# Kernel optimization log

Hardware: AMD Instinct MI355X
Metric: run time of the kernel (lower is better)

Reference implementation:

```python
import jax, jax.numpy as jnp
import numpy as np

DIM = 1024
HEADS = 16
HEAD_DIM = DIM // HEADS
SCALE = HEAD_DIM ** -0.5


def setup_inputs() -> dict:
    key = jax.random.key(0)
    ks = jax.random.split(key, 5)
    B, N, C = 2, 2048, DIM
    x = jax.random.normal(ks[0], (B, N, C), dtype=jnp.float32)
    x2 = jax.random.normal(ks[1], (B, N, C), dtype=jnp.float32)
    # torch nn.Linear weights: [out_features, in_features], no bias (qkv_bias=False)
    s = (1.0 / C) ** 0.5
    Wq = jax.random.uniform(ks[2], (C, C), jnp.float32, -s, s)
    Wa = jax.random.uniform(ks[3], (C, C), jnp.float32, -s, s)
    Wkv = jax.random.uniform(ks[4], (2 * C, C), jnp.float32, -s, s)
    return {"x": x, "x2": x2, "Wq": Wq, "Wa": Wa, "Wkv": Wkv}


def reference(x, x2, Wq, Wa, Wkv):
    B, N, C = x.shape
    H, D = HEADS, HEAD_DIM

    def heads(t):  # [B,N,C] -> [B,H,N,D]
        return t.reshape(B, N, H, D).transpose(0, 2, 1, 3)

    q = heads(x @ Wq.T)
    A = heads(x2 @ Wa.T)
    kv = (x @ Wkv.T).reshape(B, N, 2, H, D).transpose(2, 0, 3, 1, 4)
    k, v = kv[0], kv[1]

    # cascaded double attention (dropout layers in eval mode = identity)
    ATT_q = jax.nn.softmax(jnp.einsum('bhnd,bhmd->bhnm', q, A) * SCALE, axis=-1)
    ATT_k = jax.nn.softmax(jnp.einsum('bhnd,bhmd->bhnm', A, k) * SCALE, axis=-1)
    out = jnp.einsum('bhnm,bhmd->bhnd', ATT_q,
                     jnp.einsum('bhnm,bhmd->bhnd', ATT_k, v))
    return out.transpose(0, 2, 1, 3).reshape(B, N, C)
```

## Files before the change

kernel.cpp:

```cpp
#include <hip/hip_runtime.h>

#define DIM 1024
#define HEADS 16
#define HDIM 64
#define SEQ 2048
#define SCLOG2 0.18033688011112042f

typedef __attribute__((ext_vector_type(8))) short short8;
typedef __attribute__((ext_vector_type(4))) float f32x4;
typedef __attribute__((ext_vector_type(16))) float f32x16;
typedef __attribute__((ext_vector_type(4))) int i32x4;

static __device__ __forceinline__ unsigned short f2bf(float f){
  union { float f; unsigned int u; } v; v.f = f;
  unsigned int r = v.u + 0x7fffu + ((v.u >> 16) & 1u);
  return (unsigned short)(r >> 16);
}

static __device__ __forceinline__ int cvtpk(float lo, float hi){
  int r;
  asm("v_cvt_pk_bf16_f32 %0, %1, %2" : "=v"(r) : "v"(lo), "v"(hi));
  return r;
}
static __device__ __forceinline__ void swap32(int& a, int& b){
  asm("v_permlane32_swap_b32 %0, %1" : "+v"(a), "+v"(b));
}

__device__ __forceinline__ void gl_lds16(const unsigned short* g, unsigned short* l){
  __builtin_amdgcn_global_load_lds((const __attribute__((address_space(1))) void*)g,
                                   (__attribute__((address_space(3))) void*)l, 16, 0, 0);
}

#define CAST_TOTAL 3145728

__global__ __launch_bounds__(256)
void cast_all(const float* __restrict__ x, const float* __restrict__ x2,
              const float* __restrict__ wq, const float* __restrict__ wa,
              const float* __restrict__ wkv, unsigned short* __restrict__ out)
{
  for (int i = blockIdx.x*256 + threadIdx.x; i < CAST_TOTAL; i += gridDim.x*256){
    const float* src; int off;
    if      (i < 1048576){ src = x;   off = i; }
    else if (i < 2097152){ src = x2;  off = i - 1048576; }
    else if (i < 2359296){ src = wq;  off = i - 2097152; }
    else if (i < 2621440){ src = wa;  off = i - 2359296; }
    else                 { src = wkv; off = i - 2621440; }
    float4 v = ((const float4*)src)[off];
    ushort4 o;
    o.x = f2bf(v.x); o.y = f2bf(v.y); o.z = f2bf(v.z); o.w = f2bf(v.w);
    ((ushort4*)out)[i] = o;
  }
}

#define GK 1024

__global__ __launch_bounds__(256)
void gemm_all(const unsigned short* __restrict__ xb,  const unsigned short* __restrict__ x2b,
              const unsigned short* __restrict__ Wqb, const unsigned short* __restrict__ Wab,
              const unsigned short* __restrict__ Wkvb,
              unsigned short* __restrict__ Qw, unsigned short* __restrict__ Aw,
              unsigned short* __restrict__ Kw, unsigned short* __restrict__ Vwt)
{
  __shared__ unsigned short Ald[2][128*64];
  __shared__ unsigned short Bld[2][128*64];
  const int tid  = threadIdx.x;
  const int lane = tid & 63;
  const int wid  = tid >> 6;
  const int l15 = lane & 15, l4 = lane >> 4;
  const int wm = wid >> 1, wn = wid & 1;

  const int bid = blockIdx.x;
  const unsigned short *Abuf, *Bbuf;
  int mbase, nbase, isA;
  if (bid < 768){
    int xcd = bid & 7, s = bid >> 3;
    int mb = xcd*4 + (s & 3);
    int nb = s >> 2;
    nbase = nb*128; mbase = mb*128; isA = 0;
    Abuf = xb;
    Bbuf = (nbase < 1024) ? (Wqb + (size_t)nbase*GK) : (Wkvb + (size_t)(nbase-1024)*GK);
  } else {
    int b2 = bid - 768;
    int xcd = b2 & 7, s = b2 >> 3;
    int mb = xcd*4 + (s & 3);
    int nb = s >> 2;
    nbase = nb*128; mbase = mb*128; isA = 1;
    Abuf = x2b;
    Bbuf = Wab + (size_t)nbase*GK;
  }
  const bool isV = (!isA) && (nbase >= 2048);

  const int srow = wid*32 + (lane >> 3);
  const int scol = ((lane & 7) ^ (lane >> 3)) * 8;
  const unsigned short* gA = Abuf + (size_t)(mbase + srow)*GK + scol;
  const unsigned short* gB = Bbuf + (size_t)srow*GK + scol;

  const int rsw = (l15 & 7) * 8;

  f32x4 acc[4][4];
  #pragma unroll
  for (int i=0;i<4;i++)
    #pragma unroll
    for(int j=0;j<4;j++) acc[i][j] = (f32x4){0.f,0.f,0.f,0.f};

  #pragma unroll
  for (int i=0;i<4;++i){
    gl_lds16(gA + (size_t)(i*8)*GK, &Ald[0][(wid*32 + i*8)*64]);
    gl_lds16(gB + (size_t)(i*8)*GK, &Bld[0][(wid*32 + i*8)*64]);
  }
  asm volatile("s_waitcnt vmcnt(0)" ::: "memory");
  __builtin_amdgcn_s_barrier();
  __builtin_amdgcn_sched_barrier(0);

  for (int t = 0; t < 16; ++t){
    const int cur = t & 1;
    if (t+1 < 16){
      const int nxt = cur ^ 1;
      const int kt = (t+1)*64;
      #pragma unroll
      for (int i=0;i<4;++i){
        gl_lds16(gA + (size_t)(i*8)*GK + kt, &Ald[nxt][(wid*32 + i*8)*64]);
        gl_lds16(gB + (size_t)(i*8)*GK + kt, &Bld[nxt][(wid*32 + i*8)*64]);
      }
    }
    #pragma unroll
    for (int kc = 0; kc < 2; ++kc){
      short8 af[4], bf[4];
      #pragma unroll
      for (int mt=0; mt<4; ++mt)
        af[mt] = *(const short8*)(&Ald[cur][(wm*64 + mt*16 + l15)*64 + ((kc*32 + l4*8) ^ rsw)]);
      #pragma unroll
      for (int nt=0; nt<4; ++nt)
        bf[nt] = *(const short8*)(&Bld[cur][(wn*64 + nt*16 + l15)*64 + ((kc*32 + l4*8) ^ rsw)]);
      __builtin_amdgcn_s_setprio(1);
      if (isV){
        #pragma unroll
        for (int mt=0; mt<4; ++mt)
          #pragma unroll
          for (int nt=0; nt<4; ++nt)
            acc[mt][nt] = __builtin_amdgcn_mfma_f32_16x16x32_bf16(af[mt], bf[nt], acc[mt][nt], 0,0,0);
      } else {
        #pragma unroll
        for (int mt=0; mt<4; ++mt)
          #pragma unroll
          for (int nt=0; nt<4; ++nt)
            acc[mt][nt] = __builtin_amdgcn_mfma_f32_16x16x32_bf16(bf[nt], af[mt], acc[mt][nt], 0,0,0);
      }
      __builtin_amdgcn_s_setprio(0);
    }
    asm volatile("s_waitcnt vmcnt(0)" ::: "memory");
    __builtin_amdgcn_s_barrier();
    __builtin_amdgcn_sched_barrier(0);
  }

  if (!isV){
    unsigned short* dst = isA ? Aw : (nbase < 1024 ? Qw : Kw);
    const int coff = (!isA && nbase >= 1024) ? 1024 : 0;
    const float scale = isA ? SCLOG2 : 1.0f;
    #pragma unroll
    for (int mt=0; mt<4; ++mt){
      int token = mbase + wm*64 + mt*16 + l15;
      int b = token >> 11, n = token & 2047;
      #pragma unroll
      for (int nt=0; nt<4; ++nt){
        int colb = nbase - coff + wn*64 + nt*16 + l4*4;
        int h = colb >> 6, d = colb & 63;
        ushort4 pk;
        pk.x = f2bf(acc[mt][nt][0] * scale);
        pk.y = f2bf(acc[mt][nt][1] * scale);
        pk.z = f2bf(acc[mt][nt][2] * scale);
        pk.w = f2bf(acc[mt][nt][3] * scale);
        *(ushort4*)(dst + ((size_t)((b*HEADS + h)*SEQ + n))*HDIM + d) = pk;
      }
    }
  } else {
    #pragma unroll
    for (int mt=0; mt<4; ++mt){
      int mrow = mbase + wm*64 + mt*16 + l4*4;
      int b = mrow >> 11, nblk = mrow & 2047;
      #pragma unroll
      for (int nt=0; nt<4; ++nt){
        int col = nbase + wn*64 + nt*16 + l15;
        int c2 = col - 2048, h = c2 >> 6, d = c2 & 63;
        ushort4 pk;
        pk.x = f2bf(acc[mt][nt][0]);
        pk.y = f2bf(acc[mt][nt][1]);
        pk.z = f2bf(acc[mt][nt][2]);
        pk.w = f2bf(acc[mt][nt][3]);
        *(ushort4*)(Vwt + ((size_t)((b*HEADS + h)*HDIM + d))*SEQ + nblk) = pk;
      }
    }
  }
}

#define KT2 32
#define NTH 32

__global__ __launch_bounds__(512)
void attn_pass(const unsigned short* __restrict__ Qb,
               const unsigned short* __restrict__ Kb,
               const unsigned short* __restrict__ Vtb,
               unsigned short* __restrict__ ytb,
               float* __restrict__ outf,
               int mode)
{
  __shared__ __align__(16) char SHRAW[65536];
  unsigned short* SH = (unsigned short*)SHRAW;
  const int tid = threadIdx.x, lane = tid & 63, wid = tid >> 6;
  const int l31 = lane & 31, l5 = lane >> 5;
  const int qw = wid & 3, kvh = wid >> 2;

  const int bid = blockIdx.x;
  const int cx = bid & 7, j = bid >> 3;
  const int bh = cx*4 + (j >> 4);
  const int qb = j & 15;
  const int q0 = qb*128 + qw*32;
  const size_t base = (size_t)bh * SEQ * HDIM;

  short8 qf[4];
  #pragma unroll
  for (int db=0; db<4; ++db)
    qf[db] = *(const short8*)(Qb + base + (size_t)(q0 + l31)*HDIM + db*16 + l5*8);

  const unsigned short* gsrc[2];
  int ldst[2];
  int sstep;
  const int grpoff = kvh * 16384;
  if (qw < 2){
    #pragma unroll
    for (int f=0; f<2; ++f){
      gsrc[f] = Kb + base + (size_t)(kvh*1024 + l31)*HDIM + (qw*2 + f)*16 + l5*8;
      ldst[f] = grpoff + (qw*2 + f)*512;
    }
    sstep = KT2*HDIM;
  } else {
    const int db2 = qw - 2;
    #pragma unroll
    for (int f=0; f<2; ++f){
      gsrc[f] = Vtb + base + (size_t)(db2*32 + l31)*SEQ + kvh*1024 + f*16 + l5*8;
      ldst[f] = grpoff + 2048 + (db2*2 + f)*512;
    }
    sstep = KT2;
  }

  f32x16 oo0, oo1, ssum;
  #pragma unroll
  for (int r=0;r<16;++r){ oo0[r]=0.f; oo1[r]=0.f; ssum[r]=0.f; }
  short8 ones;
  #pragma unroll
  for (int jj=0;jj<8;++jj) ones[jj] = (short)0x3F80;

  #pragma unroll
  for (int b=0; b<3; ++b)
    #pragma unroll
    for (int f=0; f<2; ++f)
      gl_lds16(gsrc[f] + (size_t)b*sstep, SH + ldst[f] + b*4096);
  asm volatile("s_waitcnt vmcnt(4)" ::: "memory");
  __builtin_amdgcn_s_barrier();
  __builtin_amdgcn_sched_barrier(0);

  for (int t = 0; t < NTH; ++t){
    if (t+3 < NTH){
      const int pb = ((t+3) & 3) * 4096;
      #pragma unroll
      for (int f=0; f<2; ++f)
        gl_lds16(gsrc[f] + (size_t)(t+3)*sstep, SH + ldst[f] + pb);
    }
    const unsigned short* Kc = SH + grpoff + (t & 3)*4096;
    const unsigned short* Vc = Kc + 2048;

    f32x16 sacc;
    #pragma unroll
    for (int r=0;r<16;++r) sacc[r]=0.f;
    __builtin_amdgcn_s_setprio(1);
    #pragma unroll
    for (int db=0; db<4; ++db){
      short8 kfr = *(const short8*)(Kc + db*512 + lane*8);
      sacc = __builtin_amdgcn_mfma_f32_32x32x16_bf16(kfr, qf[db], sacc, 0,0,0);
    }
    __builtin_amdgcn_s_setprio(0);
    float p[16];
    #pragma unroll
    for (int r=0;r<16;++r)
      p[r] = __builtin_amdgcn_exp2f(sacc[r]);

    #pragma unroll
    for (int kb2=0; kb2<2; ++kb2){
      const int pb2 = kb2*8;
      int a0 = cvtpk(p[pb2+0], p[pb2+1]);
      int b0 = cvtpk(p[pb2+4], p[pb2+5]);
      int a1 = cvtpk(p[pb2+2], p[pb2+3]);
      int b1 = cvtpk(p[pb2+6], p[pb2+7]);
      swap32(a0, b0);
      swap32(a1, b1);
      i32x4 pav; pav[0]=a0; pav[1]=a1; pav[2]=b0; pav[3]=b1;
      short8 paf = *(short8*)&pav;
      __builtin_amdgcn_s_setprio(1);
      ssum = __builtin_amdgcn_mfma_f32_32x32x16_bf16(ones, paf, ssum, 0,0,0);
      short8 v0 = *(const short8*)(Vc + (0*2+kb2)*512 + lane*8);
      oo0 = __builtin_amdgcn_mfma_f32_32x32x16_bf16(v0, paf, oo0, 0,0,0);
      short8 v1 = *(const short8*)(Vc + (1*2+kb2)*512 + lane*8);
      oo1 = __builtin_amdgcn_mfma_f32_32x32x16_bf16(v1, paf, oo1, 0,0,0);
      __builtin_amdgcn_s_setprio(0);
    }

    if (t < NTH-3){
      asm volatile("s_waitcnt vmcnt(4)" ::: "memory");
    } else if (t == NTH-3){
      asm volatile("s_waitcnt vmcnt(2)" ::: "memory");
    } else if (t == NTH-2){
      asm volatile("s_waitcnt vmcnt(0)" ::: "memory");
    }
    __builtin_amdgcn_s_barrier();
    __builtin_amdgcn_sched_barrier(0);
  }

  float* Of  = (float*)SHRAW;
  float* Os1 = (float*)(SHRAW + 128*68*4);
  const int ql = qw*32 + l31;

  if (kvh == 1){
    #pragma unroll
    for (int g=0; g<4; ++g){
      f32x4 w0, w1;
      #pragma unroll
      for (int r=0;r<4;++r){ w0[r] = oo0[g*4+r]; w1[r] = oo1[g*4+r]; }
      int d0 = 8*g + 4*l5;
      *(f32x4*)(Of + ql*68 + d0)      = w0;
      *(f32x4*)(Of + ql*68 + d0 + 32) = w1;
    }
    Os1[ql] = ssum[0];
  }
  __syncthreads();

  if (kvh == 0){
    const float rinv = 1.0f / (ssum[0] + Os1[ql]);
    if (mode == 0){
      #pragma unroll
      for (int r=0;r<16;++r){
        int d0 = (r&3) + 8*(r>>2) + 4*l5;
        float f0 = (oo0[r] + Of[ql*68 + d0])      * rinv;
        float f1 = (oo1[r] + Of[ql*68 + d0 + 32]) * rinv;
        ytb[base + (size_t)(d0)*SEQ + q0 + l31]    = f2bf(f0);
        ytb[base + (size_t)(d0+32)*SEQ + q0 + l31] = f2bf(f1);
      }
    } else {
      #pragma unroll
      for (int g=0; g<4; ++g){
        int d0 = 8*g + 4*l5;
        f32x4 w0 = *(const f32x4*)(Of + ql*68 + d0);
        f32x4 w1 = *(const f32x4*)(Of + ql*68 + d0 + 32);
        #pragma unroll
        for (int r=0;r<4;++r){ w0[r] = (w0[r]+oo0[g*4+r])*rinv; w1[r] = (w1[r]+oo1[g*4+r])*rinv; }
        *(f32x4*)(Of + ql*68 + d0)      = w0;
        *(f32x4*)(Of + ql*68 + d0 + 32) = w1;
      }
    }
  }

  if (mode == 1){
    __syncthreads();
    const int b = bh >> 4, h = bh & 15;
    const int qr = tid >> 2, dh = (tid & 3)*16;
    const float* src = Of + qr*68 + dh;
    float* drow = outf + ((size_t)(b*SEQ + qb*128 + qr))*DIM + h*HDIM + dh;
    #pragma unroll
    for (int k2=0;k2<4;++k2)
      *(float4*)(drow + k2*4) = *(const float4*)(src + k2*4);
  }
}

extern "C" void kernel_launch(void* const* d_in, const int* in_sizes, int n_in,
                              void* d_out, int out_size, void* d_ws, size_t ws_size,
                              hipStream_t stream) {
  const float* x   = (const float*)d_in[0];
  const float* x2  = (const float*)d_in[1];
  const float* Wq  = (const float*)d_in[2];
  const float* Wa  = (const float*)d_in[3];
  const float* Wkv = (const float*)d_in[4];
  float* out = (float*)d_out;

  unsigned short* ws = (unsigned short*)d_ws;
  unsigned short* xb   = ws;
  unsigned short* x2b  = xb   + 4096*1024;
  unsigned short* Wqb  = x2b  + 4096*1024;
  unsigned short* Wab  = Wqb  + 1024*1024;
  unsigned short* Wkvb = Wab  + 1024*1024;
  unsigned short* Qw   = Wkvb + 2048*1024;
  unsigned short* Aw   = Qw   + 4194304;
  unsigned short* Kw   = Aw   + 4194304;
  unsigned short* Vwt  = Kw   + 4194304;
  unsigned short* Ywt  = xb;

  cast_all<<<dim3(3072), dim3(256), 0, stream>>>(x, x2, Wq, Wa, Wkv, ws);

  gemm_all<<<dim3(1024), dim3(256), 0, stream>>>(xb, x2b, Wqb, Wab, Wkvb, Qw, Aw, Kw, Vwt);

  attn_pass<<<dim3(512), dim3(512), 0, stream>>>(Aw, Kw, Vwt, Ywt, nullptr, 0);

  attn_pass<<<dim3(512), dim3(512), 0, stream>>>(Qw, Aw, Ywt, nullptr, out, 1);
}
```

Before: 149.0 us.

## Software-pipeline QK^T one tile ahead and replace ones-MFMA rowsum with VALU adds

Restructures the attention inner loop so the QK^T MFMA for tile t+1 is issued while exp2 and the PV MFMAs of tile t proceed, using two ping-pong score accumulators and a macro-unrolled pair of iterations. The row-sum MFMA against a ones vector is replaced with scalar float accumulation plus a cross-half shuffle, removing a third of the PV-phase MFMAs. Prefetch depth drops from three tiles ahead to two to fit the new schedule. This is meant to hide softmax latency behind matrix work, at the cost of more live registers, a shallower load pipeline, and a row sum taken from fp32 values rather than bf16-rounded ones.

```diff
diff --git a/kernel.cpp b/kernel.cpp
--- a/kernel.cpp
+++ b/kernel.cpp
@@ -196,6 +196,51 @@
 #define KT2 32
 #define NTH 32
 
+#define ATTN_BODY(T, SCUR, SNEXT)                                                     \
+  {                                                                                   \
+    const int t_ = (T);                                                               \
+    if (t_+2 < NTH){                                                                  \
+      const int pb_ = ((t_+2) & 3) * 4096;                                            \
+      gl_lds16(gsrc[0] + (size_t)(t_+2)*sstep, SH + ldst[0] + pb_);                   \
+      gl_lds16(gsrc[1] + (size_t)(t_+2)*sstep, SH + ldst[1] + pb_);                   \
+    }                                                                                 \
+    float p_[16];                                                                     \
+    _Pragma("unroll")                                                                 \
+    for (int r=0;r<16;++r){ p_[r] = __builtin_amdgcn_exp2f(SCUR[r]); os[r&3] += p_[r]; } \
+    if (t_+2 < NTH){ asm volatile("s_waitcnt vmcnt(2)" ::: "memory"); }               \
+    else if (t_+1 < NTH){ asm volatile("s_waitcnt vmcnt(0)" ::: "memory"); }          \
+    __builtin_amdgcn_s_barrier();                                                     \
+    __builtin_amdgcn_sched_barrier(0);                                                \
+    const unsigned short* Kc_ = SH + grpoff + ((t_+1) & 3)*4096;                      \
+    const unsigned short* Vc_ = SH + grpoff + (t_ & 3)*4096 + 2048;                   \
+    __builtin_amdgcn_s_setprio(1);                                                    \
+    if (t_+1 < NTH){                                                                  \
+      _Pragma("unroll")                                                               \
+      for (int r=0;r<16;++r) SNEXT[r]=0.f;                                            \
+      _Pragma("unroll")                                                               \
+      for (int db=0; db<4; ++db){                                                     \
+        short8 kfr = *(const short8*)(Kc_ + db*512 + lane*8);                         \
+        SNEXT = __builtin_amdgcn_mfma_f32_32x32x16_bf16(kfr, qf[db], SNEXT, 0,0,0);   \
+      }                                                                               \
+    }                                                                                 \
+    _Pragma("unroll")                                                                 \
+    for (int kb2=0; kb2<2; ++kb2){                                                    \
+      const int pb2 = kb2*8;                                                          \
+      int a0 = cvtpk(p_[pb2+0], p_[pb2+1]);                                           \
+      int b0 = cvtpk(p_[pb2+4], p_[pb2+5]);                                           \
+      int a1 = cvtpk(p_[pb2+2], p_[pb2+3]);                                           \
+      int b1 = cvtpk(p_[pb2+6], p_[pb2+7]);                                           \
+      swap32(a0, b0); swap32(a1, b1);                                                 \
+      i32x4 pav; pav[0]=a0; pav[1]=a1; pav[2]=b0; pav[3]=b1;                          \
+      short8 paf = *(short8*)&pav;                                                    \
+      short8 v0 = *(const short8*)(Vc_ + (0*2+kb2)*512 + lane*8);                     \
+      oo0 = __builtin_amdgcn_mfma_f32_32x32x16_bf16(v0, paf, oo0, 0,0,0);             \
+      short8 v1 = *(const short8*)(Vc_ + (1*2+kb2)*512 + lane*8);                     \
+      oo1 = __builtin_amdgcn_mfma_f32_32x32x16_bf16(v1, paf, oo1, 0,0,0);             \
+    }                                                                                 \
+    __builtin_amdgcn_s_setprio(0);                                                    \
+  }
+
 __global__ __launch_bounds__(512)
 void attn_pass(const unsigned short* __restrict__ Qb,
                const unsigned short* __restrict__ Kb,
@@ -243,77 +288,40 @@
     sstep = KT2;
   }
 
-  f32x16 oo0, oo1, ssum;
+  f32x16 oo0, oo1;
   #pragma unroll
-  for (int r=0;r<16;++r){ oo0[r]=0.f; oo1[r]=0.f; ssum[r]=0.f; }
-  short8 ones;
+  for (int r=0;r<16;++r){ oo0[r]=0.f; oo1[r]=0.f; }
+  float os[4] = {0.f, 0.f, 0.f, 0.f};
+
   #pragma unroll
-  for (int jj=0;jj<8;++jj) ones[jj] = (short)0x3F80;
-
-  #pragma unroll
-  for (int b=0; b<3; ++b)
-    #pragma unroll
-    for (int f=0; f<2; ++f)
-      gl_lds16(gsrc[f] + (size_t)b*sstep, SH + ldst[f] + b*4096);
-  asm volatile("s_waitcnt vmcnt(4)" ::: "memory");
+  for (int b=0; b<2; ++b){
+    gl_lds16(gsrc[0] + (size_t)b*sstep, SH + ldst[0] + b*4096);
+    gl_lds16(gsrc[1] + (size_t)b*sstep, SH + ldst[1] + b*4096);
+  }
+  asm volatile("s_waitcnt vmcnt(2)" ::: "memory");
   __builtin_amdgcn_s_barrier();
   __builtin_amdgcn_sched_barrier(0);
 
-  for (int t = 0; t < NTH; ++t){
-    if (t+3 < NTH){
-      const int pb = ((t+3) & 3) * 4096;
-      #pragma unroll
-      for (int f=0; f<2; ++f)
-        gl_lds16(gsrc[f] + (size_t)(t+3)*sstep, SH + ldst[f] + pb);
-    }
-    const unsigned short* Kc = SH + grpoff + (t & 3)*4096;
-    const unsigned short* Vc = Kc + 2048;
-
-    f32x16 sacc;
-    #pragma unroll
-    for (int r=0;r<16;++r) sacc[r]=0.f;
-    __builtin_amdgcn_s_setprio(1);
+  f32x16 sA, sB;
+  {
+    #pragma unroll
+    for (int r=0;r<16;++r) sA[r]=0.f;
+    const unsigned short* Kc0 = SH + grpoff;
     #pragma unroll
     for (int db=0; db<4; ++db){
-      short8 kfr = *(const short8*)(Kc + db*512 + lane*8);
-      sacc = __builtin_amdgcn_mfma_f32_32x32x16_bf16(kfr, qf[db], sacc, 0,0,0);
-    }
-    __builtin_amdgcn_s_setprio(0);
-    float p[16];
-    #pragma unroll
-    for (int r=0;r<16;++r)
-      p[r] = __builtin_amdgcn_exp2f(sacc[r]);
-
-    #pragma unroll
-    for (int kb2=0; kb2<2; ++kb2){
-      const int pb2 = kb2*8;
-      int a0 = cvtpk(p[pb2+0], p[pb2+1]);
-      int b0 = cvtpk(p[pb2+4], p[pb2+5]);
-      int a1 = cvtpk(p[pb2+2], p[pb2+3]);
-      int b1 = cvtpk(p[pb2+6], p[pb2+7]);
-      swap32(a0, b0);
-      swap32(a1, b1);
-      i32x4 pav; pav[0]=a0; pav[1]=a1; pav[2]=b0; pav[3]=b1;
-      short8 paf = *(short8*)&pav;
-      __builtin_amdgcn_s_setprio(1);
-      ssum = __builtin_amdgcn_mfma_f32_32x32x16_bf16(ones, paf, ssum, 0,0,0);
-      short8 v0 = *(const short8*)(Vc + (0*2+kb2)*512 + lane*8);
-      oo0 = __builtin_amdgcn_mfma_f32_32x32x16_bf16(v0, paf, oo0, 0,0,0);
-      short8 v1 = *(const short8*)(Vc + (1*2+kb2)*512 + lane*8);
-      oo1 = __builtin_amdgcn_mfma_f32_32x32x16_bf16(v1, paf, oo1, 0,0,0);
-      __builtin_amdgcn_s_setprio(0);
-    }
-
-    if (t < NTH-3){
-      asm volatile("s_waitcnt vmcnt(4)" ::: "memory");
-    } else if (t == NTH-3){
-      asm volatile("s_waitcnt vmcnt(2)" ::: "memory");
-    } else if (t == NTH-2){
-      asm volatile("s_waitcnt vmcnt(0)" ::: "memory");
-    }
-    __builtin_amdgcn_s_barrier();
-    __builtin_amdgcn_sched_barrier(0);
-  }
+      short8 kfr = *(const short8*)(Kc0 + db*512 + lane*8);
+      sA = __builtin_amdgcn_mfma_f32_32x32x16_bf16(kfr, qf[db], sA, 0,0,0);
+    }
+  }
+
+  for (int tt = 0; tt < NTH; tt += 2){
+    ATTN_BODY(tt,   sA, sB);
+    ATTN_BODY(tt+1, sB, sA);
+  }
+  __syncthreads();
+
+  float osum = (os[0]+os[1]) + (os[2]+os[3]);
+  osum += __shfl_xor(osum, 32);
 
   float* Of  = (float*)SHRAW;
   float* Os1 = (float*)(SHRAW + 128*68*4);
@@ -329,12 +337,12 @@
       *(f32x4*)(Of + ql*68 + d0)      = w0;
       *(f32x4*)(Of + ql*68 + d0 + 32) = w1;
     }
-    Os1[ql] = ssum[0];
+    Os1[ql] = osum;
   }
   __syncthreads();
 
   if (kvh == 0){
-    const float rinv = 1.0f / (ssum[0] + Os1[ql]);
+    const float rinv = 1.0f / (osum + Os1[ql]);
     if (mode == 0){
       #pragma unroll
       for (int r=0;r<16;++r){
```

After: 154.9 us. 4.0% more time.

## Pair-buffer KV tiles and replace ones-MFMA row sum with VALU accumulation

Applied to the files above, without the earlier changes.

Replaces the 4-slot ring with per-tile barriers by a double buffer of tile pairs, processing two KV tiles per barrier and prefetching the next pair while computing. The softmax denominator is now accumulated with VALU adds plus one cross-lane shuffle, instead of an extra MFMA against a ones vector. This removes one of three PV-stage MFMAs and halves the barrier count. In exchange, prefetch depth shrinks and each pair ends with a full vmcnt(0) wait, which may expose global-load latency. The VALU sum also uses fp32 probabilities rather than the bf16-rounded values the MFMA summed.

```diff
diff --git a/kernel.cpp b/kernel.cpp
--- a/kernel.cpp
+++ b/kernel.cpp
@@ -243,77 +243,82 @@
     sstep = KT2;
   }
 
-  f32x16 oo0, oo1, ssum;
+  f32x16 oo0, oo1;
   #pragma unroll
-  for (int r=0;r<16;++r){ oo0[r]=0.f; oo1[r]=0.f; ssum[r]=0.f; }
-  short8 ones;
+  for (int r=0;r<16;++r){ oo0[r]=0.f; oo1[r]=0.f; }
+  float os[4] = {0.f, 0.f, 0.f, 0.f};
+
   #pragma unroll
-  for (int jj=0;jj<8;++jj) ones[jj] = (short)0x3F80;
-
-  #pragma unroll
-  for (int b=0; b<3; ++b)
+  for (int b=0; b<2; ++b)
     #pragma unroll
     for (int f=0; f<2; ++f)
       gl_lds16(gsrc[f] + (size_t)b*sstep, SH + ldst[f] + b*4096);
-  asm volatile("s_waitcnt vmcnt(4)" ::: "memory");
+  asm volatile("s_waitcnt vmcnt(0)" ::: "memory");
   __builtin_amdgcn_s_barrier();
   __builtin_amdgcn_sched_barrier(0);
 
-  for (int t = 0; t < NTH; ++t){
-    if (t+3 < NTH){
-      const int pb = ((t+3) & 3) * 4096;
-      #pragma unroll
-      for (int f=0; f<2; ++f)
-        gl_lds16(gsrc[f] + (size_t)(t+3)*sstep, SH + ldst[f] + pb);
-    }
-    const unsigned short* Kc = SH + grpoff + (t & 3)*4096;
-    const unsigned short* Vc = Kc + 2048;
-
-    f32x16 sacc;
-    #pragma unroll
-    for (int r=0;r<16;++r) sacc[r]=0.f;
-    __builtin_amdgcn_s_setprio(1);
-    #pragma unroll
-    for (int db=0; db<4; ++db){
-      short8 kfr = *(const short8*)(Kc + db*512 + lane*8);
-      sacc = __builtin_amdgcn_mfma_f32_32x32x16_bf16(kfr, qf[db], sacc, 0,0,0);
-    }
-    __builtin_amdgcn_s_setprio(0);
-    float p[16];
-    #pragma unroll
-    for (int r=0;r<16;++r)
-      p[r] = __builtin_amdgcn_exp2f(sacc[r]);
-
-    #pragma unroll
-    for (int kb2=0; kb2<2; ++kb2){
-      const int pb2 = kb2*8;
-      int a0 = cvtpk(p[pb2+0], p[pb2+1]);
-      int b0 = cvtpk(p[pb2+4], p[pb2+5]);
-      int a1 = cvtpk(p[pb2+2], p[pb2+3]);
-      int b1 = cvtpk(p[pb2+6], p[pb2+7]);
-      swap32(a0, b0);
-      swap32(a1, b1);
-      i32x4 pav; pav[0]=a0; pav[1]=a1; pav[2]=b0; pav[3]=b1;
-      short8 paf = *(short8*)&pav;
+  for (int i = 0; i < 16; ++i){
+    const int pairBase = (i & 1) * 8192;
+    if (i < 15){
+      const int stBase = pairBase ^ 8192;
+      #pragma unroll
+      for (int u=0; u<2; ++u)
+        #pragma unroll
+        for (int f=0; f<2; ++f)
+          gl_lds16(gsrc[f] + (size_t)(2*i+2+u)*sstep, SH + ldst[f] + stBase + u*4096);
+    }
+
+    #pragma unroll
+    for (int u=0; u<2; ++u){
+      const unsigned short* Kc = SH + grpoff + pairBase + u*4096;
+      const unsigned short* Vc = Kc + 2048;
+
+      f32x16 sacc;
+      #pragma unroll
+      for (int r=0;r<16;++r) sacc[r]=0.f;
       __builtin_amdgcn_s_setprio(1);
-      ssum = __builtin_amdgcn_mfma_f32_32x32x16_bf16(ones, paf, ssum, 0,0,0);
-      short8 v0 = *(const short8*)(Vc + (0*2+kb2)*512 + lane*8);
-      oo0 = __builtin_amdgcn_mfma_f32_32x32x16_bf16(v0, paf, oo0, 0,0,0);
-      short8 v1 = *(const short8*)(Vc + (1*2+kb2)*512 + lane*8);
-      oo1 = __builtin_amdgcn_mfma_f32_32x32x16_bf16(v1, paf, oo1, 0,0,0);
+      #pragma unroll
+      for (int db=0; db<4; ++db){
+        short8 kfr = *(const short8*)(Kc + db*512 + lane*8);
+        sacc = __builtin_amdgcn_mfma_f32_32x32x16_bf16(kfr, qf[db], sacc, 0,0,0);
+      }
       __builtin_amdgcn_s_setprio(0);
-    }
-
-    if (t < NTH-3){
-      asm volatile("s_waitcnt vmcnt(4)" ::: "memory");
-    } else if (t == NTH-3){
-      asm volatile("s_waitcnt vmcnt(2)" ::: "memory");
-    } else if (t == NTH-2){
+      float p[16];
+      #pragma unroll
+      for (int r=0;r<16;++r){
+        p[r] = __builtin_amdgcn_exp2f(sacc[r]);
+        os[r & 3] += p[r];
+      }
+
+      #pragma unroll
+      for (int kb2=0; kb2<2; ++kb2){
+        const int pb2 = kb2*8;
+        int a0 = cvtpk(p[pb2+0], p[pb2+1]);
+        int b0 = cvtpk(p[pb2+4], p[pb2+5]);
+        int a1 = cvtpk(p[pb2+2], p[pb2+3]);
+        int b1 = cvtpk(p[pb2+6], p[pb2+7]);
+        swap32(a0, b0);
+        swap32(a1, b1);
+        i32x4 pav; pav[0]=a0; pav[1]=a1; pav[2]=b0; pav[3]=b1;
+        short8 paf = *(short8*)&pav;
+        __builtin_amdgcn_s_setprio(1);
+        short8 v0 = *(const short8*)(Vc + (0*2+kb2)*512 + lane*8);
+        oo0 = __builtin_amdgcn_mfma_f32_32x32x16_bf16(v0, paf, oo0, 0,0,0);
+        short8 v1 = *(const short8*)(Vc + (1*2+kb2)*512 + lane*8);
+        oo1 = __builtin_amdgcn_mfma_f32_32x32x16_bf16(v1, paf, oo1, 0,0,0);
+        __builtin_amdgcn_s_setprio(0);
+      }
+    }
+
+    if (i < 15){
       asm volatile("s_waitcnt vmcnt(0)" ::: "memory");
     }
     __builtin_amdgcn_s_barrier();
     __builtin_amdgcn_sched_barrier(0);
   }
+
+  float osum = (os[0]+os[1]) + (os[2]+os[3]);
+  osum += __shfl_xor(osum, 32);
 
   float* Of  = (float*)SHRAW;
   float* Os1 = (float*)(SHRAW + 128*68*4);
@@ -329,12 +334,12 @@
       *(f32x4*)(Of + ql*68 + d0)      = w0;
       *(f32x4*)(Of + ql*68 + d0 + 32) = w1;
     }
-    Os1[ql] = ssum[0];
+    Os1[ql] = osum;
   }
   __syncthreads();
 
   if (kvh == 0){
-    const float rinv = 1.0f / (ssum[0] + Os1[ql]);
+    const float rinv = 1.0f / (osum + Os1[ql]);
     if (mode == 0){
       #pragma unroll
       for (int r=0;r<16;++r){
```

Measured after the change: 146.8 us (median of 3 runs). About the same (-1.5%).
